# Performance work log

Hardware: AMD Instinct MI355X
Metric: run time of the kernel (lower is better)

Reference implementation:

```python
import jax, jax.numpy as jnp
import numpy as np

B, IN, H, A, K = 8192, 2048, 256, 8192, 512

def setup_inputs() -> dict:
    key = jax.random.key(0)
    ks = jax.random.split(key, 8)
    s1, s2, s3 = 1.0/np.sqrt(IN), 1.0/np.sqrt(H), 1.0/np.sqrt(H)
    return {
        "x": jax.random.normal(ks[0], (B, IN), dtype=jnp.float32),
        "possible_moves": jax.random.randint(ks[1], (B, K), 0, A, dtype=jnp.int64),
        "W1": jax.random.uniform(ks[2], (IN, H), jnp.float32, -s1, s1),
        "b1": jax.random.uniform(ks[3], (H,), jnp.float32, -s1, s1),
        "W2": jax.random.uniform(ks[4], (H, H), jnp.float32, -s2, s2),
        "b2": jax.random.uniform(ks[5], (H,), jnp.float32, -s2, s2),
        "W3": jax.random.uniform(ks[6], (H, A), jnp.float32, -s3, s3),
        "b3": jax.random.uniform(ks[7], (A,), jnp.float32, -s3, s3),
    }

def reference(x, possible_moves, W1, b1, W2, b2, W3, b3):
    h = jax.nn.relu(x @ W1 + b1)
    h = jax.nn.relu(h @ W2 + b2)
    q = h @ W3 + b3                      # [B, A]
    # build per-sample legal-move mask via scatter (replaces torch python loop)
    rows = jnp.arange(q.shape[0])[:, None]
    mask = jnp.zeros(q.shape, q.dtype).at[rows, possible_moves].set(1.0)
    filtered = q * mask
    # faithful to torch: any exact-zero entry (illegal OR q==0) becomes -inf
    return jnp.where(filtered == 0, -jnp.inf, filtered)
```

## Files before the change

kernel.cpp:

```cpp
#include <hip/hip_runtime.h>
#include <math.h>
#include <stdint.h>

#define B_DIM   8192
#define IN_DIM  2048
#define H_DIM   256
#define A_DIM   8192
#define K_MOVES 512

#define NEG_SENTINEL (-3.0e38f)

typedef __attribute__((ext_vector_type(8))) short          short8;
typedef __attribute__((ext_vector_type(8))) unsigned short ushort8;
typedef __attribute__((ext_vector_type(4))) unsigned short ushort4v;
typedef __attribute__((ext_vector_type(4))) float          f32x4;

#define MFMA_16x16x32_BF16(a, b, c) \
    __builtin_amdgcn_mfma_f32_16x16x32_bf16((a), (b), (c), 0, 0, 0)

__device__ __forceinline__ unsigned short f2bf(float f) {
    union { float f; unsigned int u; } v; v.f = f;
    unsigned int r = v.u + 0x7fffu + ((v.u >> 16) & 1u);
    return (unsigned short)(r >> 16);
}

__device__ __forceinline__ ushort8 pack8(float4 a, float4 b) {
    ushort8 o;
    o[0] = f2bf(a.x); o[1] = f2bf(a.y); o[2] = f2bf(a.z); o[3] = f2bf(a.w);
    o[4] = f2bf(b.x); o[5] = f2bf(b.y); o[6] = f2bf(b.z); o[7] = f2bf(b.w);
    return o;
}

__global__ __launch_bounds__(256)
void scatter_mask_kernel(const int* __restrict__ pm,
                         unsigned long long* __restrict__ mask) {
    __shared__ unsigned long long lm[A_DIM / 64];
    const int row = blockIdx.x;
    const int tid = threadIdx.x;
    if (tid < 128) lm[tid] = 0ULL;
    __syncthreads();
    const int* p = pm + (size_t)row * K_MOVES;
#pragma unroll
    for (int s = 0; s < K_MOVES / 256; ++s) {
        int mv = p[s * 256 + tid];
        if (mv < 0) mv = 0;
        if (mv >= A_DIM) mv = A_DIM - 1;
        atomicOr(&lm[mv >> 6], 1ULL << (mv & 63));
    }
    __syncthreads();
    if (tid < 128) mask[(size_t)row * 128 + tid] = lm[tid];
}

__global__ __launch_bounds__(256)
void transpose3_kernel(const float* __restrict__ W1, unsigned short* __restrict__ W1t,
                       const float* __restrict__ W2, unsigned short* __restrict__ W2t,
                       const float* __restrict__ W3, unsigned short* __restrict__ W3t) {
    __shared__ unsigned short tile[32][33];
    const int bid = blockIdx.x;
    const float* in; unsigned short* out; int R, C, bx, by;
    if (bid < 512)      { in = W1; out = W1t; R = IN_DIM; C = H_DIM;
                          bx = bid % 8;          by = bid / 8; }
    else if (bid < 576) { in = W2; out = W2t; R = H_DIM;  C = H_DIM;
                          int t = bid - 512; bx = t % 8;   by = t / 8; }
    else                { in = W3; out = W3t; R = H_DIM;  C = A_DIM;
                          int t = bid - 576; bx = t % 256; by = t / 256; }
    const int tx = threadIdx.x, ty = threadIdx.y;
    int x = bx * 32 + tx;
#pragma unroll
    for (int i = 0; i < 32; i += 8) {
        int y = by * 32 + ty + i;
        tile[ty + i][tx] = f2bf(in[(size_t)y * C + x]);
    }
    __syncthreads();
    int ox = by * 32 + tx;
#pragma unroll
    for (int i = 0; i < 32; i += 8) {
        int oy = bx * 32 + ty + i;
        out[(size_t)oy * R + ox] = tile[tx][ty + i];
    }
}

template <typename AT>
__global__ __launch_bounds__(256)
void gemm_small(const AT* __restrict__ A,
                const unsigned short* __restrict__ Bt,
                const float* __restrict__ bias,
                unsigned short* __restrict__ C,
                int M, int N, int K) {
    constexpr bool A_F32 = (sizeof(AT) == 4);
    constexpr int LDA = 72;
    __shared__ __align__(16) unsigned short As[64 * LDA];
    __shared__ __align__(16) unsigned short Bs[64 * LDA];

    const int tid  = threadIdx.x;
    const int wave = tid >> 6, lane = tid & 63;
    const int quad = lane >> 4, tl = lane & 15;
    const int wm = wave >> 1,  wn = wave & 1;
    const int row0 = blockIdx.y * 64, col0 = blockIdx.x * 64;
    const int sr = tid >> 2;
    const int sk = (tid & 3) * 16;

    f32x4 acc[2][2];
#pragma unroll
    for (int i = 0; i < 2; ++i)
#pragma unroll
        for (int j = 0; j < 2; ++j) acc[i][j] = {0.f, 0.f, 0.f, 0.f};

    const AT* Ap             = A  + (size_t)(row0 + sr) * K + sk;
    const unsigned short* Bp = Bt + (size_t)(col0 + sr) * K + sk;

    float4  pa[4];
    ushort8 pa8[2];
    ushort8 pb[2];

    if constexpr (A_F32) {
#pragma unroll
        for (int q = 0; q < 4; ++q) pa[q] = ((const float4*)Ap)[q];
    } else {
        pa8[0] = ((const ushort8*)Ap)[0];
        pa8[1] = ((const ushort8*)Ap)[1];
    }
    pb[0] = ((const ushort8*)Bp)[0];
    pb[1] = ((const ushort8*)Bp)[1];

    const int iters = K >> 6;
    for (int t = 0; t < iters; ++t) {
        if constexpr (A_F32) {
            *(ushort8*)&As[sr * LDA + sk]     = pack8(pa[0], pa[1]);
            *(ushort8*)&As[sr * LDA + sk + 8] = pack8(pa[2], pa[3]);
        } else {
            *(ushort8*)&As[sr * LDA + sk]     = pa8[0];
            *(ushort8*)&As[sr * LDA + sk + 8] = pa8[1];
        }
        *(ushort8*)&Bs[sr * LDA + sk]     = pb[0];
        *(ushort8*)&Bs[sr * LDA + sk + 8] = pb[1];
        __syncthreads();

        if (t + 1 < iters) {
            const AT* ap             = Ap + (t + 1) * 64;
            const unsigned short* bp = Bp + (t + 1) * 64;
            if constexpr (A_F32) {
#pragma unroll
                for (int q = 0; q < 4; ++q) pa[q] = ((const float4*)ap)[q];
            } else {
                pa8[0] = ((const ushort8*)ap)[0];
                pa8[1] = ((const ushort8*)ap)[1];
            }
            pb[0] = ((const ushort8*)bp)[0];
            pb[1] = ((const ushort8*)bp)[1];
        }

#pragma unroll
        for (int ks = 0; ks < 2; ++ks) {
            short8 af[2], bf[2];
#pragma unroll
            for (int i = 0; i < 2; ++i)
                af[i] = *(const short8*)&As[(wm * 32 + i * 16 + tl) * LDA + ks * 32 + quad * 8];
#pragma unroll
            for (int j = 0; j < 2; ++j)
                bf[j] = *(const short8*)&Bs[(wn * 32 + j * 16 + tl) * LDA + ks * 32 + quad * 8];
#pragma unroll
            for (int i = 0; i < 2; ++i)
#pragma unroll
                for (int j = 0; j < 2; ++j)
                    acc[i][j] = MFMA_16x16x32_BF16(bf[j], af[i], acc[i][j]);
        }
        __syncthreads();
    }

    float4 bj4[2];
#pragma unroll
    for (int j = 0; j < 2; ++j)
        bj4[j] = *(const float4*)&bias[col0 + wn * 32 + j * 16 + quad * 4];
#pragma unroll
    for (int i = 0; i < 2; ++i) {
        const int r = row0 + wm * 32 + i * 16 + tl;
#pragma unroll
        for (int j = 0; j < 2; ++j) {
            ushort4v o;
#pragma unroll
            for (int reg = 0; reg < 4; ++reg) {
                float q = acc[i][j][reg] + ((const float*)&bj4[j])[reg];
                o[reg] = f2bf(fmaxf(q, 0.f));
            }
            *(ushort4v*)&C[(size_t)r * N + col0 + wn * 32 + j * 16 + quad * 4] = o;
        }
    }
}

__global__ __launch_bounds__(512)
void gemm3_once(const unsigned short* __restrict__ A,
                const unsigned short* __restrict__ Bt,
                const float* __restrict__ bias,
                float* __restrict__ C,
                const unsigned long long* __restrict__ mask) {
    constexpr int K = H_DIM;
    constexpr int N = A_DIM;
    __shared__ __align__(16) unsigned short Bs[8 * 128 * 32];

    const int tid  = threadIdx.x;
    const int wave = tid >> 6, lane = tid & 63;
    const int quad = lane >> 4, tl = lane & 15;
    const int row0 = blockIdx.y * 256, col0 = blockIdx.x * 128;

#pragma unroll
    for (int p = 0; p < 8; ++p) {
        const int L  = p * 512 + tid;
        const int c4 = L & 3, n = (L >> 2) & 127, s = L >> 9;
        const unsigned short* g = Bt + (size_t)(col0 + n) * K + s * 32 + c4 * 8;
        __builtin_amdgcn_global_load_lds(
            (const __attribute__((address_space(1))) void*)g,
            (__attribute__((address_space(3))) void*)&Bs[(p * 512 + wave * 64) * 8],
            16, 0, 0);
    }

    const int rw0 = row0 + wave * 32;
    short8 af[2][8];
#pragma unroll
    for (int i = 0; i < 2; ++i)
#pragma unroll
        for (int s = 0; s < 8; ++s)
            af[i][s] = *(const short8*)&A[(size_t)(rw0 + i * 16 + tl) * K + s * 32 + quad * 8];

    unsigned long long mw[2][2];
#pragma unroll
    for (int i = 0; i < 2; ++i) {
        const size_t r = rw0 + i * 16 + tl;
        mw[i][0] = mask[r * (N >> 6) + (col0 >> 6)];
        mw[i][1] = mask[r * (N >> 6) + (col0 >> 6) + 1];
    }

    __syncthreads();

#pragma unroll
    for (int jj = 0; jj < 8; ++jj) {
        short8 bf[8];
#pragma unroll
        for (int s = 0; s < 8; ++s)
            bf[s] = *(const short8*)&Bs[((s * 128) + jj * 16 + tl) * 32 + quad * 8];

        const float4 b4 = *(const float4*)&bias[col0 + jj * 16 + quad * 4];

#pragma unroll
        for (int i = 0; i < 2; ++i) {
            f32x4 acc = {b4.x, b4.y, b4.z, b4.w};
#pragma unroll
            for (int s = 0; s < 8; ++s)
                acc = MFMA_16x16x32_BF16(bf[s], af[i][s], acc);

            const int r = rw0 + i * 16 + tl;
            const unsigned long long w = mw[i][jj >> 2];
            float q[4];
#pragma unroll
            for (int reg = 0; reg < 4; ++reg) {
                float v = acc[reg];
                const int bit = (jj & 3) * 16 + quad * 4 + reg;
                bool legal = (w >> bit) & 1ULL;
                bool ok = legal && (v != 0.f) && (fabsf(v) < 1.0e30f);
                q[reg] = ok ? v : NEG_SENTINEL;
            }
            *(float4*)&C[(size_t)r * N + col0 + jj * 16 + quad * 4] =
                make_float4(q[0], q[1], q[2], q[3]);
        }
    }
}

extern "C" void kernel_launch(void* const* d_in, const int* in_sizes, int n_in,
                              void* d_out, int out_size, void* d_ws, size_t ws_size,
                              hipStream_t stream) {
    const float* x  = (const float*)d_in[0];
    const int*   pm = (const int*)d_in[1];
    const float* W1 = (const float*)d_in[2];
    const float* b1 = (const float*)d_in[3];
    const float* W2 = (const float*)d_in[4];
    const float* b2 = (const float*)d_in[5];
    const float* W3 = (const float*)d_in[6];
    const float* b3 = (const float*)d_in[7];
    float* out = (float*)d_out;

    char* ws = (char*)d_ws;
    unsigned long long* mask = (unsigned long long*)ws;
    unsigned short* W1t = (unsigned short*)(ws + (8ull  << 20));
    unsigned short* W2t = (unsigned short*)(ws + (9ull  << 20));
    unsigned short* W3t = (unsigned short*)(ws + (10ull << 20));
    unsigned short* h1b = (unsigned short*)(ws + (16ull << 20));
    unsigned short* h2b = (unsigned short*)(ws + (20ull << 20));

    transpose3_kernel<<<2624, dim3(32, 8), 0, stream>>>(W1, W1t, W2, W2t, W3, W3t);

    scatter_mask_kernel<<<B_DIM, 256, 0, stream>>>(pm, mask);

    gemm_small<float><<<dim3(H_DIM / 64, B_DIM / 64), 256, 0, stream>>>(
        x, W1t, b1, h1b, B_DIM, H_DIM, IN_DIM);

    gemm_small<unsigned short><<<dim3(H_DIM / 64, B_DIM / 64), 256, 0, stream>>>(
        h1b, W2t, b2, h2b, B_DIM, H_DIM, H_DIM);

    gemm3_once<<<dim3(A_DIM / 128, B_DIM / 256), 512, 0, stream>>>(
        h2b, W3t, b3, out, mask);
}
```

Measured before the change: 434.9 us.

## Fuse all stages into one persistent kernel with grid barriers

Replaces the five kernel launches (weight transpose, mask scatter, two small GEMMs, output GEMM) with one persistent 256-block kernel that runs the phases in order, separated by software grid barriers on an atomic counter. The two small GEMMs are reworked so each block owns a 32-row strip with the full 256 columns, and the final GEMM loops over 16 column tiles per block instead of using a 2D grid. The goal is to remove launch gaps and inter-kernel tails. In exchange, parallelism drops to 256 blocks, the grid barriers add spinning, and correctness depends on all blocks being co-resident.

```diff
diff --git a/kernel.cpp b/kernel.cpp
--- a/kernel.cpp
+++ b/kernel.cpp
@@ -7,6 +7,7 @@
 #define H_DIM   256
 #define A_DIM   8192
 #define K_MOVES 512
+#define NBLK    256
 
 #define NEG_SENTINEL (-3.0e38f)
 
@@ -18,249 +19,232 @@
 #define MFMA_16x16x32_BF16(a, b, c) \
     __builtin_amdgcn_mfma_f32_16x16x32_bf16((a), (b), (c), 0, 0, 0)
 
+#define LGKM_BARRIER() asm volatile("s_waitcnt lgkmcnt(0)\n\ts_barrier" ::: "memory")
+
 __device__ __forceinline__ unsigned short f2bf(float f) {
     union { float f; unsigned int u; } v; v.f = f;
     unsigned int r = v.u + 0x7fffu + ((v.u >> 16) & 1u);
     return (unsigned short)(r >> 16);
 }
-
-__device__ __forceinline__ ushort8 pack8(float4 a, float4 b) {
-    ushort8 o;
+__device__ __forceinline__ ushort4v pack4(float4 a) {
+    ushort4v o;
     o[0] = f2bf(a.x); o[1] = f2bf(a.y); o[2] = f2bf(a.z); o[3] = f2bf(a.w);
-    o[4] = f2bf(b.x); o[5] = f2bf(b.y); o[6] = f2bf(b.z); o[7] = f2bf(b.w);
     return o;
 }
 
-__global__ __launch_bounds__(256)
-void scatter_mask_kernel(const int* __restrict__ pm,
-                         unsigned long long* __restrict__ mask) {
-    __shared__ unsigned long long lm[A_DIM / 64];
-    const int row = blockIdx.x;
-    const int tid = threadIdx.x;
-    if (tid < 128) lm[tid] = 0ULL;
+__device__ __forceinline__ void grid_barrier(unsigned int* bar, int idx, int tid) {
     __syncthreads();
-    const int* p = pm + (size_t)row * K_MOVES;
-#pragma unroll
-    for (int s = 0; s < K_MOVES / 256; ++s) {
-        int mv = p[s * 256 + tid];
-        if (mv < 0) mv = 0;
-        if (mv >= A_DIM) mv = A_DIM - 1;
-        atomicOr(&lm[mv >> 6], 1ULL << (mv & 63));
+    if (tid == 0) {
+        __threadfence();
+        atomicAdd(&bar[idx], 1u);
+        while (__hip_atomic_load(&bar[idx], __ATOMIC_ACQUIRE,
+                                 __HIP_MEMORY_SCOPE_AGENT) < NBLK)
+            __builtin_amdgcn_s_sleep(2);
+        __threadfence();
     }
     __syncthreads();
-    if (tid < 128) mask[(size_t)row * 128 + tid] = lm[tid];
-}
-
-__global__ __launch_bounds__(256)
-void transpose3_kernel(const float* __restrict__ W1, unsigned short* __restrict__ W1t,
-                       const float* __restrict__ W2, unsigned short* __restrict__ W2t,
-                       const float* __restrict__ W3, unsigned short* __restrict__ W3t) {
-    __shared__ unsigned short tile[32][33];
-    const int bid = blockIdx.x;
-    const float* in; unsigned short* out; int R, C, bx, by;
-    if (bid < 512)      { in = W1; out = W1t; R = IN_DIM; C = H_DIM;
-                          bx = bid % 8;          by = bid / 8; }
-    else if (bid < 576) { in = W2; out = W2t; R = H_DIM;  C = H_DIM;
-                          int t = bid - 512; bx = t % 8;   by = t / 8; }
-    else                { in = W3; out = W3t; R = H_DIM;  C = A_DIM;
-                          int t = bid - 576; bx = t % 256; by = t / 256; }
-    const int tx = threadIdx.x, ty = threadIdx.y;
-    int x = bx * 32 + tx;
-#pragma unroll
-    for (int i = 0; i < 32; i += 8) {
-        int y = by * 32 + ty + i;
-        tile[ty + i][tx] = f2bf(in[(size_t)y * C + x]);
-    }
-    __syncthreads();
-    int ox = by * 32 + tx;
-#pragma unroll
-    for (int i = 0; i < 32; i += 8) {
-        int oy = bx * 32 + ty + i;
-        out[(size_t)oy * R + ox] = tile[tx][ty + i];
-    }
 }
 
 template <typename AT>
-__global__ __launch_bounds__(256)
-void gemm_small(const AT* __restrict__ A,
-                const unsigned short* __restrict__ Bt,
-                const float* __restrict__ bias,
-                unsigned short* __restrict__ C,
-                int M, int N, int K) {
+__device__ __forceinline__ void gemm12(const AT* __restrict__ A,
+                                       const unsigned short* __restrict__ Bt,
+                                       const float* __restrict__ bias,
+                                       unsigned short* __restrict__ Cout,
+                                       int K, int row0,
+                                       unsigned short* As, unsigned short* Bs,
+                                       int tid) {
     constexpr bool A_F32 = (sizeof(AT) == 4);
     constexpr int LDA = 72;
-    __shared__ __align__(16) unsigned short As[64 * LDA];
-    __shared__ __align__(16) unsigned short Bs[64 * LDA];
-
-    const int tid  = threadIdx.x;
     const int wave = tid >> 6, lane = tid & 63;
     const int quad = lane >> 4, tl = lane & 15;
-    const int wm = wave >> 1,  wn = wave & 1;
-    const int row0 = blockIdx.y * 64, col0 = blockIdx.x * 64;
-    const int sr = tid >> 2;
-    const int sk = (tid & 3) * 16;
-
-    f32x4 acc[2][2];
-#pragma unroll
-    for (int i = 0; i < 2; ++i)
-#pragma unroll
-        for (int j = 0; j < 2; ++j) acc[i][j] = {0.f, 0.f, 0.f, 0.f};
-
-    const AT* Ap             = A  + (size_t)(row0 + sr) * K + sk;
-    const unsigned short* Bp = Bt + (size_t)(col0 + sr) * K + sk;
-
-    float4  pa[4];
-    ushort8 pa8[2];
-    ushort8 pb[2];
-
-    if constexpr (A_F32) {
-#pragma unroll
-        for (int q = 0; q < 4; ++q) pa[q] = ((const float4*)Ap)[q];
-    } else {
-        pa8[0] = ((const ushort8*)Ap)[0];
-        pa8[1] = ((const ushort8*)Ap)[1];
-    }
-    pb[0] = ((const ushort8*)Bp)[0];
-    pb[1] = ((const ushort8*)Bp)[1];
+    const int wm = wave >> 2, wn = wave & 3;
+    const int sra = tid >> 4,  ska = (tid & 15) * 4;
+    const int srb = tid >> 1,  skb = (tid & 1) * 32;
+
+    f32x4 acc[4];
+#pragma unroll
+    for (int j = 0; j < 4; ++j) acc[j] = {0.f, 0.f, 0.f, 0.f};
+
+    const AT* Ap             = A  + (size_t)(row0 + sra) * K + ska;
+    const unsigned short* Bp = Bt + (size_t)srb * K + skb;
+
+    float4   paf; ushort4v pau;
+    ushort8  pb[4];
+    if constexpr (A_F32) paf = *(const float4*)Ap;
+    else                 pau = *(const ushort4v*)Ap;
+#pragma unroll
+    for (int q = 0; q < 4; ++q) pb[q] = ((const ushort8*)Bp)[q];
 
     const int iters = K >> 6;
     for (int t = 0; t < iters; ++t) {
-        if constexpr (A_F32) {
-            *(ushort8*)&As[sr * LDA + sk]     = pack8(pa[0], pa[1]);
-            *(ushort8*)&As[sr * LDA + sk + 8] = pack8(pa[2], pa[3]);
-        } else {
-            *(ushort8*)&As[sr * LDA + sk]     = pa8[0];
-            *(ushort8*)&As[sr * LDA + sk + 8] = pa8[1];
-        }
-        *(ushort8*)&Bs[sr * LDA + sk]     = pb[0];
-        *(ushort8*)&Bs[sr * LDA + sk + 8] = pb[1];
+        if constexpr (A_F32) *(ushort4v*)&As[sra * LDA + ska] = pack4(paf);
+        else                 *(ushort4v*)&As[sra * LDA + ska] = pau;
+#pragma unroll
+        for (int q = 0; q < 4; ++q)
+            *(ushort8*)&Bs[srb * LDA + skb + 8 * q] = pb[q];
         __syncthreads();
 
         if (t + 1 < iters) {
             const AT* ap             = Ap + (t + 1) * 64;
             const unsigned short* bp = Bp + (t + 1) * 64;
-            if constexpr (A_F32) {
-#pragma unroll
-                for (int q = 0; q < 4; ++q) pa[q] = ((const float4*)ap)[q];
-            } else {
-                pa8[0] = ((const ushort8*)ap)[0];
-                pa8[1] = ((const ushort8*)ap)[1];
-            }
-            pb[0] = ((const ushort8*)bp)[0];
-            pb[1] = ((const ushort8*)bp)[1];
+            if constexpr (A_F32) paf = *(const float4*)ap;
+            else                 pau = *(const ushort4v*)ap;
+#pragma unroll
+            for (int q = 0; q < 4; ++q) pb[q] = ((const ushort8*)bp)[q];
         }
 
 #pragma unroll
         for (int ks = 0; ks < 2; ++ks) {
-            short8 af[2], bf[2];
-#pragma unroll
-            for (int i = 0; i < 2; ++i)
-                af[i] = *(const short8*)&As[(wm * 32 + i * 16 + tl) * LDA + ks * 32 + quad * 8];
-#pragma unroll
-            for (int j = 0; j < 2; ++j)
-                bf[j] = *(const short8*)&Bs[(wn * 32 + j * 16 + tl) * LDA + ks * 32 + quad * 8];
-#pragma unroll
-            for (int i = 0; i < 2; ++i)
-#pragma unroll
-                for (int j = 0; j < 2; ++j)
-                    acc[i][j] = MFMA_16x16x32_BF16(bf[j], af[i], acc[i][j]);
+            short8 af = *(const short8*)&As[(wm * 16 + tl) * LDA + ks * 32 + quad * 8];
+#pragma unroll
+            for (int j = 0; j < 4; ++j) {
+                short8 bf = *(const short8*)&Bs[(wn * 64 + j * 16 + tl) * LDA + ks * 32 + quad * 8];
+                acc[j] = MFMA_16x16x32_BF16(bf, af, acc[j]);
+            }
         }
         __syncthreads();
     }
 
-    float4 bj4[2];
-#pragma unroll
-    for (int j = 0; j < 2; ++j)
-        bj4[j] = *(const float4*)&bias[col0 + wn * 32 + j * 16 + quad * 4];
-#pragma unroll
-    for (int i = 0; i < 2; ++i) {
-        const int r = row0 + wm * 32 + i * 16 + tl;
-#pragma unroll
-        for (int j = 0; j < 2; ++j) {
-            ushort4v o;
-#pragma unroll
-            for (int reg = 0; reg < 4; ++reg) {
-                float q = acc[i][j][reg] + ((const float*)&bj4[j])[reg];
-                o[reg] = f2bf(fmaxf(q, 0.f));
-            }
-            *(ushort4v*)&C[(size_t)r * N + col0 + wn * 32 + j * 16 + quad * 4] = o;
-        }
-    }
-}
-
-__global__ __launch_bounds__(512)
-void gemm3_once(const unsigned short* __restrict__ A,
-                const unsigned short* __restrict__ Bt,
-                const float* __restrict__ bias,
-                float* __restrict__ C,
-                const unsigned long long* __restrict__ mask) {
-    constexpr int K = H_DIM;
-    constexpr int N = A_DIM;
-    __shared__ __align__(16) unsigned short Bs[8 * 128 * 32];
-
-    const int tid  = threadIdx.x;
-    const int wave = tid >> 6, lane = tid & 63;
-    const int quad = lane >> 4, tl = lane & 15;
-    const int row0 = blockIdx.y * 256, col0 = blockIdx.x * 128;
-
-#pragma unroll
-    for (int p = 0; p < 8; ++p) {
-        const int L  = p * 512 + tid;
-        const int c4 = L & 3, n = (L >> 2) & 127, s = L >> 9;
-        const unsigned short* g = Bt + (size_t)(col0 + n) * K + s * 32 + c4 * 8;
-        __builtin_amdgcn_global_load_lds(
-            (const __attribute__((address_space(1))) void*)g,
-            (__attribute__((address_space(3))) void*)&Bs[(p * 512 + wave * 64) * 8],
-            16, 0, 0);
-    }
-
-    const int rw0 = row0 + wave * 32;
-    short8 af[2][8];
-#pragma unroll
-    for (int i = 0; i < 2; ++i)
+    const int r = row0 + wm * 16 + tl;
+#pragma unroll
+    for (int j = 0; j < 4; ++j) {
+        const int c = wn * 64 + j * 16 + quad * 4;
+        const float4 b4 = *(const float4*)&bias[c];
+        ushort4v o;
+#pragma unroll
+        for (int reg = 0; reg < 4; ++reg)
+            o[reg] = f2bf(fmaxf(acc[j][reg] + ((const float*)&b4)[reg], 0.f));
+        *(ushort4v*)&Cout[(size_t)r * H_DIM + c] = o;
+    }
+}
+
+__global__ __launch_bounds__(512, 2)
+void mega_kernel(const float* __restrict__ x, const int* __restrict__ pm,
+                 const float* __restrict__ W1, const float* __restrict__ b1,
+                 const float* __restrict__ W2, const float* __restrict__ b2,
+                 const float* __restrict__ W3, const float* __restrict__ b3,
+                 float* __restrict__ out,
+                 unsigned long long* __restrict__ mask,
+                 unsigned short* __restrict__ W1t,
+                 unsigned short* __restrict__ W2t,
+                 unsigned short* __restrict__ W3t,
+                 unsigned short* __restrict__ h1b,
+                 unsigned short* __restrict__ h2b,
+                 unsigned int* __restrict__ bar) {
+    __shared__ __align__(16) unsigned char smem[65536];
+    const int tid = threadIdx.x;
+    const int bid = blockIdx.x;
+
+    {
+        unsigned short* tile = (unsigned short*)smem + (tid >> 8) * 1152;
+        const int grp = tid >> 8, ltid = tid & 255;
+        const int tx = ltid & 31, ty = ltid >> 5;
+        for (int it = 0; it < 6; ++it) {
+            const int j = it * 512 + bid * 2 + grp;
+            const bool act = j < 2624;
+            const float* in = nullptr; unsigned short* op = nullptr;
+            int R = 0, C = 0, bx = 0, by = 0;
+            if (act) {
+                if (j < 512)      { in = W1; op = W1t; R = IN_DIM; C = H_DIM;
+                                    bx = j & 7;          by = j >> 3; }
+                else if (j < 576) { in = W2; op = W2t; R = H_DIM;  C = H_DIM;
+                                    int t = j - 512; bx = t & 7;   by = t >> 3; }
+                else              { in = W3; op = W3t; R = H_DIM;  C = A_DIM;
+                                    int t = j - 576; bx = t & 255; by = t >> 8; }
+#pragma unroll
+                for (int i = 0; i < 32; i += 8)
+                    tile[(ty + i) * 33 + tx] =
+                        f2bf(in[(size_t)(by * 32 + ty + i) * C + bx * 32 + tx]);
+            }
+            __syncthreads();
+            if (act) {
+#pragma unroll
+                for (int i = 0; i < 32; i += 8)
+                    op[(size_t)(bx * 32 + ty + i) * R + by * 32 + tx] =
+                        tile[tx * 33 + ty + i];
+            }
+            __syncthreads();
+        }
+        unsigned long long* lm = (unsigned long long*)smem;
+        for (int rr = 0; rr < 32; ++rr) {
+            const int row = bid * 32 + rr;
+            if (tid < 128) lm[tid] = 0ULL;
+            __syncthreads();
+            int mv = pm[(size_t)row * K_MOVES + tid];
+            if (mv < 0) mv = 0;
+            if (mv >= A_DIM) mv = A_DIM - 1;
+            atomicOr(&lm[mv >> 6], 1ULL << (mv & 63));
+            __syncthreads();
+            if (tid < 128) mask[(size_t)row * 128 + tid] = lm[tid];
+            __syncthreads();
+        }
+    }
+    grid_barrier(bar, 0, tid);
+
+    {
+        unsigned short* As = (unsigned short*)smem;
+        unsigned short* Bs = (unsigned short*)(smem + 4608);
+        gemm12<float>(x, W1t, b1, h1b, IN_DIM, bid * 32, As, Bs, tid);
+        __syncthreads();
+        gemm12<unsigned short>(h1b, W2t, b2, h2b, H_DIM, bid * 32, As, Bs, tid);
+    }
+    grid_barrier(bar, 1, tid);
+
+    {
+        unsigned short* Bs3 = (unsigned short*)smem;
+        const int wave = tid >> 6, lane = tid & 63;
+        const int quad = lane >> 4, tl = lane & 15;
+        const int by = bid >> 2, cq = bid & 3;
+        const int rw = by * 128 + wave * 16 + tl;
+
+        short8 af[8];
 #pragma unroll
         for (int s = 0; s < 8; ++s)
-            af[i][s] = *(const short8*)&A[(size_t)(rw0 + i * 16 + tl) * K + s * 32 + quad * 8];
-
-    unsigned long long mw[2][2];
-#pragma unroll
-    for (int i = 0; i < 2; ++i) {
-        const size_t r = rw0 + i * 16 + tl;
-        mw[i][0] = mask[r * (N >> 6) + (col0 >> 6)];
-        mw[i][1] = mask[r * (N >> 6) + (col0 >> 6) + 1];
-    }
-
-    __syncthreads();
-
-#pragma unroll
-    for (int jj = 0; jj < 8; ++jj) {
-        short8 bf[8];
-#pragma unroll
-        for (int s = 0; s < 8; ++s)
-            bf[s] = *(const short8*)&Bs[((s * 128) + jj * 16 + tl) * 32 + quad * 8];
-
-        const float4 b4 = *(const float4*)&bias[col0 + jj * 16 + quad * 4];
-
-#pragma unroll
-        for (int i = 0; i < 2; ++i) {
-            f32x4 acc = {b4.x, b4.y, b4.z, b4.w};
-#pragma unroll
-            for (int s = 0; s < 8; ++s)
-                acc = MFMA_16x16x32_BF16(bf[s], af[i][s], acc);
-
-            const int r = rw0 + i * 16 + tl;
-            const unsigned long long w = mw[i][jj >> 2];
-            float q[4];
-#pragma unroll
-            for (int reg = 0; reg < 4; ++reg) {
-                float v = acc[reg];
-                const int bit = (jj & 3) * 16 + quad * 4 + reg;
-                bool legal = (w >> bit) & 1ULL;
-                bool ok = legal && (v != 0.f) && (fabsf(v) < 1.0e30f);
-                q[reg] = ok ? v : NEG_SENTINEL;
-            }
-            *(float4*)&C[(size_t)r * N + col0 + jj * 16 + quad * 4] =
-                make_float4(q[0], q[1], q[2], q[3]);
+            af[s] = *(const short8*)&h2b[(size_t)rw * H_DIM + s * 32 + quad * 8];
+
+        for (int i = 0; i < 16; ++i) {
+            const int col0 = (cq * 16 + i) * 128;
+#pragma unroll
+            for (int p = 0; p < 8; ++p) {
+                const int L = p * 512 + tid;
+                const int c4 = L & 3, n = (L >> 2) & 127, s = L >> 9;
+                const unsigned short* g =
+                    W3t + (size_t)(col0 + n) * H_DIM + s * 32 + c4 * 8;
+                __builtin_amdgcn_global_load_lds(
+                    (const __attribute__((address_space(1))) void*)g,
+                    (__attribute__((address_space(3))) void*)&Bs3[(p * 512 + wave * 64) * 8],
+                    16, 0, 0);
+            }
+            const unsigned long long mw0 = mask[(size_t)rw * 128 + (col0 >> 6)];
+            const unsigned long long mw1 = mask[(size_t)rw * 128 + (col0 >> 6) + 1];
+            __syncthreads();
+
+#pragma unroll
+            for (int jj = 0; jj < 8; ++jj) {
+                short8 bf[8];
+#pragma unroll
+                for (int s = 0; s < 8; ++s)
+                    bf[s] = *(const short8*)&Bs3[(s * 128 + jj * 16 + tl) * 32 + quad * 8];
+                const float4 b4 = *(const float4*)&b3[col0 + jj * 16 + quad * 4];
+                f32x4 acc = {b4.x, b4.y, b4.z, b4.w};
+#pragma unroll
+                for (int s = 0; s < 8; ++s)
+                    acc = MFMA_16x16x32_BF16(bf[s], af[s], acc);
+
+                const unsigned long long w = (jj >> 2) ? mw1 : mw0;
+                float q[4];
+#pragma unroll
+                for (int reg = 0; reg < 4; ++reg) {
+                    float v = acc[reg];
+                    const int bit = (jj & 3) * 16 + quad * 4 + reg;
+                    bool legal = (w >> bit) & 1ULL;
+                    bool ok = legal && (v != 0.f) && (fabsf(v) < 1.0e30f);
+                    q[reg] = ok ? v : NEG_SENTINEL;
+                }
+                *(float4*)&out[(size_t)rw * A_DIM + col0 + jj * 16 + quad * 4] =
+                    make_float4(q[0], q[1], q[2], q[3]);
+            }
+            LGKM_BARRIER();
         }
     }
 }
@@ -285,17 +269,11 @@
     unsigned short* W3t = (unsigned short*)(ws + (10ull << 20));
     unsigned short* h1b = (unsigned short*)(ws + (16ull << 20));
     unsigned short* h2b = (unsigned short*)(ws + (20ull << 20));
-
-    transpose3_kernel<<<2624, dim3(32, 8), 0, stream>>>(W1, W1t, W2, W2t, W3, W3t);
-
-    scatter_mask_kernel<<<B_DIM, 256, 0, stream>>>(pm, mask);
-
-    gemm_small<float><<<dim3(H_DIM / 64, B_DIM / 64), 256, 0, stream>>>(
-        x, W1t, b1, h1b, B_DIM, H_DIM, IN_DIM);
-
-    gemm_small<unsigned short><<<dim3(H_DIM / 64, B_DIM / 64), 256, 0, stream>>>(
-        h1b, W2t, b2, h2b, B_DIM, H_DIM, H_DIM);
-
-    gemm3_once<<<dim3(A_DIM / 128, B_DIM / 256), 512, 0, stream>>>(
-        h2b, W3t, b3, out, mask);
-}
+    unsigned int*   bar = (unsigned int*)(ws + (24ull << 20));
+
+    hipMemsetAsync(bar, 0, 64, stream);
+
+    mega_kernel<<<dim3(NBLK), dim3(512), 0, stream>>>(
+        x, pm, W1, b1, W2, b2, W3, b3, out,
+        mask, W1t, W2t, W3t, h1b, h2b, bar);
+}
```

New measurement: 596.2 us. 37.1% more time.
